# Performance work log

Hardware: AMD Instinct MI355X
Metric: run time of the kernel (lower is better)

## Reference

```python
import jax, jax.numpy as jnp
import numpy as np

N_NODES = 100000
N_EDGES = 3200000
IN_FEATS = 512
HIDDEN = 256
N_CLASSES = 64
NITER = 10
HALT_BIAS_INIT = 3.0


def setup_inputs() -> dict:
    key = jax.random.key(0)
    ks = jax.random.split(key, 8)
    x = jax.random.normal(ks[0], (N_NODES, IN_FEATS), dtype=jnp.float32)
    edge_index = jax.random.randint(ks[1], (2, N_EDGES), 0, N_NODES, dtype=jnp.int64)
    # Linear layers: layers[0]: in->hidden, layers[1]: hidden->classes, halt: classes->1
    W0 = jax.random.normal(ks[2], (IN_FEATS, HIDDEN), dtype=jnp.float32) / np.sqrt(IN_FEATS)
    b0 = jnp.zeros((HIDDEN,), dtype=jnp.float32)
    W1 = jax.random.normal(ks[3], (HIDDEN, N_CLASSES), dtype=jnp.float32) / np.sqrt(HIDDEN)
    b1 = jnp.zeros((N_CLASSES,), dtype=jnp.float32)
    Wh = jax.random.normal(ks[4], (N_CLASSES, 1), dtype=jnp.float32) / np.sqrt(N_CLASSES)
    bh = jnp.full((1,), HALT_BIAS_INIT, dtype=jnp.float32)
    return {"x": x, "edge_index": edge_index, "edge_dropout": 0,
            "W0": W0, "b0": b0, "W1": W1, "b1": b1, "Wh": Wh, "bh": bh}


def reference(x, edge_index, edge_dropout, W0, b0, W1, b1, Wh, bh):
    N = x.shape[0]
    # MLP encoder (eval mode: dropout is identity)
    h = jax.nn.relu(x @ W0 + b0)
    h = h @ W1 + b1                                   # [N, C]

    # gcn_norm with self-loops (edge_dropout=0 in eval => identical every iter)
    loops = jnp.arange(N, dtype=edge_index.dtype)
    row = jnp.concatenate([edge_index[0], loops])     # source
    col = jnp.concatenate([edge_index[1], loops])     # target (aggregation index)
    deg = jax.ops.segment_sum(jnp.ones_like(col, dtype=h.dtype), col, num_segments=N)
    dinv = jnp.where(deg > 0, deg ** -0.5, 0.0)
    norm = dinv[row] * dinv[col]                      # [E+N]

    def step(ph, _):
        msg = norm[:, None] * ph[row]                 # gather + scale, [E+N, C]
        ph2 = jax.ops.segment_sum(msg, col, num_segments=N)  # scatter_add
        logit = jnp.clip(ph2 @ Wh + bh, -10.0, 10.0)  # [N, 1]
        return ph2, (ph2, logit)

    _, (props, logits) = jax.lax.scan(step, h, None, length=NITER)
    outputs = jnp.concatenate([h[None], props], axis=0)       # [niter+1, N, C]
    halting_logits = jnp.transpose(logits[:, :, 0])           # [N, niter]

    lam = jax.nn.sigmoid(halting_logits)
    remain = jnp.cumprod(1.0 - lam, axis=1)                   # inclusive
    remain_excl = jnp.concatenate([jnp.ones((N, 1), lam.dtype), remain[:, :-1]], axis=1)
    p = lam * remain_excl
    p = p.at[:, -1].add(remain[:, -1])                        # leftover mass to last step
    return outputs, p, halting_logits
```

## Files before the change

kernel.cpp:

```cpp
#include <hip/hip_runtime.h>
#include <hip/hip_bf16.h>

#define N_NODES  100000
#define N_EDGES  3200000
#define IN_FEATS 512
#define HIDDEN   256
#define N_CLASSES 64
#define NITER    10

#define SCAN_NB  49

#define OUT_P_OFF  ((size_t)(NITER + 1) * N_NODES * N_CLASSES)
#define OUT_HL_OFF (OUT_P_OFF + (size_t)N_NODES * NITER)

#define WS_META_INTS (4 * N_NODES + 128)
#define WS_CSR_OFF   ((size_t)WS_META_INTS * 4)
#define WS_W0F_OFF   (WS_CSR_OFF + (size_t)2 * N_EDGES * 4)
#define WS_W1F_OFF   (WS_W0F_OFF + 262144)
#define WS_SH0_OFF   (WS_W1F_OFF + 32768)
#define WS_SH1_OFF   (WS_SH0_OFF + (size_t)N_NODES * 64 * 2)
#define WS_NEED_W    (WS_SH0_OFF)
#define WS_NEED_BF   (WS_SH1_OFF + (size_t)N_NODES * 64 * 2)

typedef _Float16 f16x8 __attribute__((ext_vector_type(8)));
typedef _Float16 f16x4 __attribute__((ext_vector_type(4)));
typedef float    f32x4 __attribute__((ext_vector_type(4)));

__device__ __forceinline__ float bflo(unsigned v) { return __uint_as_float(v << 16); }
__device__ __forceinline__ float bfhi(unsigned v) { return __uint_as_float(v & 0xffff0000u); }
__device__ __forceinline__ unsigned short f2bf(float f) {
    unsigned u = __float_as_uint(f);
    return (unsigned short)((u + 0x7fffu + ((u >> 16) & 1u)) >> 16);
}

__global__ void k_detect(const int* ei, int* flag) {
    if (threadIdx.x == 0 && blockIdx.x == 0) {
        int is64 = 1;
        for (int k = 0; k < 128; ++k) {
            if (ei[2 * k + 1] != 0) { is64 = 0; break; }
        }
        *flag = is64;
    }
}

__device__ __forceinline__ int edge_row(const void* ei, int is64, int e) {
    return is64 ? (int)((const long long*)ei)[e] : ((const int*)ei)[e];
}
__device__ __forceinline__ int edge_col(const void* ei, int is64, int e) {
    return is64 ? (int)((const long long*)ei)[(size_t)N_EDGES + e]
                : ((const int*)ei)[(size_t)N_EDGES + e];
}

__global__ void k_count(const void* ei, const int* flag, int* cnt) {
    int e = blockIdx.x * 256 + threadIdx.x;
    if (e >= N_EDGES) return;
    int is64 = *flag;
    atomicAdd(&cnt[edge_col(ei, is64, e)], 1);
}

__global__ __launch_bounds__(256) void k_scan1(const int* cnt, int* part) {
    __shared__ int sd[256];
    int b = blockIdx.x, t = threadIdx.x;
    int s = 0;
    for (int j = t; j < 2048; j += 256) {
        int idx = b * 2048 + j;
        if (idx < N_NODES) s += cnt[idx];
    }
    sd[t] = s;
    __syncthreads();
    for (int o = 128; o > 0; o >>= 1) {
        if (t < o) sd[t] += sd[t + o];
        __syncthreads();
    }
    if (t == 0) part[b] = sd[0];
}

__global__ __launch_bounds__(256) void k_scan2(int* part, int* offs) {
    __shared__ int sd[256];
    int t = threadIdx.x;
    sd[t] = (t < SCAN_NB) ? part[t] : 0;
    __syncthreads();
    for (int o = 1; o < 256; o <<= 1) {
        int add = (t >= o) ? sd[t - o] : 0;
        __syncthreads();
        sd[t] += add;
        __syncthreads();
    }
    if (t < SCAN_NB) part[t] = (t == 0) ? 0 : sd[t - 1];
    if (t == 0) offs[N_NODES] = N_EDGES;
}

__global__ __launch_bounds__(256) void k_scan3(const int* cnt, const int* part, int* offs) {
    __shared__ int sd[256];
    int b = blockIdx.x, t = threadIdx.x;
    int base = b * 2048 + t * 8;
    int local[8];
    int s = 0;
#pragma unroll
    for (int j = 0; j < 8; ++j) {
        int idx = base + j;
        int v = (idx < N_NODES) ? cnt[idx] : 0;
        local[j] = s;
        s += v;
    }
    sd[t] = s;
    __syncthreads();
    for (int o = 1; o < 256; o <<= 1) {
        int add = (t >= o) ? sd[t - o] : 0;
        __syncthreads();
        sd[t] += add;
        __syncthreads();
    }
    int tbase = part[b] + ((t == 0) ? 0 : sd[t - 1]);
#pragma unroll
    for (int j = 0; j < 8; ++j) {
        int idx = base + j;
        if (idx < N_NODES) offs[idx] = tbase + local[j];
    }
}

__global__ void k_dinv(const int* cnt, float* dinv) {
    int i = blockIdx.x * 256 + threadIdx.x;
    if (i >= N_NODES) return;
    dinv[i] = rsqrtf((float)(cnt[i] + 1));
}

__global__ void k_fill(const void* ei, const int* flag,
                       const int* offs, int* cursor, int* csr) {
    int e = blockIdx.x * 256 + threadIdx.x;
    if (e >= N_EDGES) return;
    int is64 = *flag;
    int r = edge_row(ei, is64, e);
    int c = edge_col(ei, is64, e);
    int pos = offs[c] + atomicAdd(&cursor[c], 1);
    csr[pos] = r << 7;
}

__global__ void k_prep_w(const float* __restrict__ W0, const float* __restrict__ W1,
                         _Float16* __restrict__ W0f, _Float16* __restrict__ W1f) {
    int id = blockIdx.x * 256 + threadIdx.x;
    if (id < 16384) {
        int l = id & 63, c = (id >> 6) & 15, kkg = id >> 10;
        int n = c * 16 + (l & 15);
        int kb = kkg * 32 + ((l >> 4) * 8);
        f16x8 v;
#pragma unroll
        for (int j = 0; j < 8; ++j) v[j] = (_Float16)W0[(size_t)(kb + j) * HIDDEN + n];
        *(f16x8*)&W0f[(size_t)id * 8] = v;
    } else if (id < 16384 + 2048) {
        int id2 = id - 16384;
        int l = id2 & 63, c = (id2 >> 6) & 3, kkg = id2 >> 8;
        int n = c * 16 + (l & 15);
        int kb = kkg * 32 + ((l >> 4) * 8);
        f16x8 v;
#pragma unroll
        for (int j = 0; j < 8; ++j) v[j] = (_Float16)W1[(size_t)(kb + j) * N_CLASSES + n];
        *(f16x8*)&W1f[(size_t)id2 * 8] = v;
    }
}

#define EBM 64
#define XS_STRIDE 72
#define H1_STRIDE 264
#define XS0   0
#define XS1   9216
#define WST0  18432
#define WST1  34816
#define W2ST0 34816
#define W2ST1 38912
__global__ __launch_bounds__(256) void k_encoder_mfma(
        const float* __restrict__ x, const _Float16* __restrict__ W0f,
        const float* __restrict__ b0, const _Float16* __restrict__ W1f,
        const float* __restrict__ b1, float* __restrict__ out,
        const float* __restrict__ dinv,
        unsigned short* __restrict__ shadow, int write_shadow) {
    __shared__ char smem[51200];
    const int t = threadIdx.x;
    const int w = t >> 6, l = t & 63;
    const int g = l >> 4, r15 = l & 15;
    const int row0 = blockIdx.x * EBM;
    const int c4 = t & 15;
    const int srow0 = t >> 4;

    f32x4 acc[16];
#pragma unroll
    for (int c = 0; c < 16; ++c) acc[c] = (f32x4){0.f, 0.f, 0.f, 0.f};

    float4 xld[4];
    f16x8 wld[4];
#pragma unroll
    for (int q = 0; q < 4; ++q) {
        int grow = row0 + q * 16 + srow0;
        if (grow >= N_NODES) grow = N_NODES - 1;
        xld[q] = *(const float4*)&x[(size_t)grow * IN_FEATS + c4 * 4];
    }
#pragma unroll
    for (int q = 0; q < 4; ++q) wld[q] = *(const f16x8*)&W0f[(size_t)(q * 256 + t) * 8];
#pragma unroll
    for (int q = 0; q < 4; ++q) {
        f16x4 hv = {(_Float16)xld[q].x, (_Float16)xld[q].y, (_Float16)xld[q].z, (_Float16)xld[q].w};
        *(f16x4*)(smem + XS0 + ((q * 16 + srow0) * XS_STRIDE + c4 * 4) * 2) = hv;
    }
#pragma unroll
    for (int q = 0; q < 4; ++q)
        *(f16x8*)(smem + WST0 + (q * 256 + t) * 16) = wld[q];
    __syncthreads();

    for (int kkg = 0; kkg < 16; ++kkg) {
        const int kc = kkg >> 1, kk = kkg & 1;
        if (kkg < 15) {
#pragma unroll
            for (int q = 0; q < 4; ++q)
                wld[q] = *(const f16x8*)&W0f[(size_t)((kkg + 1) * 1024 + q * 256 + t) * 8];
        }
        if (kk == 0 && kc < 7) {
#pragma unroll
            for (int q = 0; q < 4; ++q) {
                int grow = row0 + q * 16 + srow0;
                if (grow >= N_NODES) grow = N_NODES - 1;
                xld[q] = *(const float4*)&x[(size_t)grow * IN_FEATS + (kc + 1) * 64 + c4 * 4];
            }
        }
        const char* xbase = smem + ((kc & 1) ? XS1 : XS0);
        const char* wbase = smem + ((kkg & 1) ? WST1 : WST0);
        f16x8 af = *(const f16x8*)(xbase + ((w * 16 + r15) * XS_STRIDE + kk * 32 + g * 8) * 2);
#pragma unroll
        for (int c = 0; c < 16; ++c) {
            f16x8 bf = *(const f16x8*)(wbase + ((c << 6) | l) * 16);
            acc[c] = __builtin_amdgcn_mfma_f32_16x16x32_f16(af, bf, acc[c], 0, 0, 0);
        }
        if (kkg < 15) {
            char* wdst = smem + ((kkg & 1) ? WST0 : WST1);
#pragma unroll
            for (int q = 0; q < 4; ++q)
                *(f16x8*)(wdst + (q * 256 + t) * 16) = wld[q];
        }
        if (kk == 1 && kc < 7) {
            char* xdst = smem + ((kc & 1) ? XS0 : XS1);
#pragma unroll
            for (int q = 0; q < 4; ++q) {
                f16x4 hv = {(_Float16)xld[q].x, (_Float16)xld[q].y, (_Float16)xld[q].z, (_Float16)xld[q].w};
                *(f16x4*)(xdst + ((q * 16 + srow0) * XS_STRIDE + c4 * 4) * 2) = hv;
            }
        }
        __syncthreads();
    }

    f16x8 w2ld = *(const f16x8*)&W1f[(size_t)t * 8];
#pragma unroll
    for (int c = 0; c < 16; ++c) {
        float bb = b0[c * 16 + r15];
#pragma unroll
        for (int i = 0; i < 4; ++i) {
            int row = w * 16 + g * 4 + i;
            *(_Float16*)(smem + (row * H1_STRIDE + c * 16 + r15) * 2) =
                (_Float16)fmaxf(acc[c][i] + bb, 0.f);
        }
    }
    *(f16x8*)(smem + W2ST0 + t * 16) = w2ld;
    __syncthreads();

    f32x4 acc2[4];
#pragma unroll
    for (int c = 0; c < 4; ++c) acc2[c] = (f32x4){0.f, 0.f, 0.f, 0.f};
    for (int kkg = 0; kkg < 8; ++kkg) {
        if (kkg < 7) w2ld = *(const f16x8*)&W1f[(size_t)((kkg + 1) * 256 + t) * 8];
        const char* wbase = smem + ((kkg & 1) ? W2ST1 : W2ST0);
        f16x8 af = *(const f16x8*)(smem + ((w * 16 + r15) * H1_STRIDE + kkg * 32 + g * 8) * 2);
#pragma unroll
        for (int c = 0; c < 4; ++c) {
            f16x8 bf = *(const f16x8*)(wbase + ((c << 6) | l) * 16);
            acc2[c] = __builtin_amdgcn_mfma_f32_16x16x32_f16(af, bf, acc2[c], 0, 0, 0);
        }
        if (kkg < 7)
            *(f16x8*)(smem + ((kkg & 1) ? W2ST0 : W2ST1) + t * 16) = w2ld;
        __syncthreads();
    }
#pragma unroll
    for (int c = 0; c < 4; ++c) {
        float bb = b1[c * 16 + r15];
#pragma unroll
        for (int i = 0; i < 4; ++i) {
            int row = row0 + w * 16 + g * 4 + i;
            if (row < N_NODES) {
                float v = acc2[c][i] + bb;
                int col = c * 16 + r15;
                out[(size_t)row * 64 + col] = v;
                if (write_shadow)
                    shadow[(size_t)row * 64 + col] = f2bf(dinv[row] * v);
            }
        }
    }
}

__global__ __launch_bounds__(256) void k_encoder(const float* __restrict__ x,
        const float* __restrict__ W0, const float* __restrict__ b0,
        const float* __restrict__ W1, const float* __restrict__ b1,
        float* __restrict__ out) {
    __shared__ float xsh[32][128];
    __shared__ float h1s[32][HIDDEN + 1];
    const int t = threadIdx.x;
    const int rg = t >> 6;
    const int cg = t & 63;
    const size_t row0 = (size_t)blockIdx.x * 32;
    float acc[8][4];
#pragma unroll
    for (int i = 0; i < 8; ++i)
        acc[i][0] = acc[i][1] = acc[i][2] = acc[i][3] = 0.f;
    for (int kc = 0; kc < 4; ++kc) {
        __syncthreads();
#pragma unroll
        for (int q = 0; q < 4; ++q) {
            int idx = t + q * 256;
            int r = idx >> 5, pos = idx & 31;
            *(float4*)&xsh[r][pos * 4] =
                *(const float4*)&x[(row0 + r) * IN_FEATS + kc * 128 + pos * 4];
        }
        __syncthreads();
        for (int kk = 0; kk < 128; kk += 4) {
            float4 xv[8];
#pragma unroll
            for (int i = 0; i < 8; ++i) xv[i] = *(const float4*)&xsh[rg * 8 + i][kk];
#pragma unroll
            for (int j = 0; j < 4; ++j) {
                float4 wv = *(const float4*)&W0[(size_t)(kc * 128 + kk + j) * HIDDEN + cg * 4];
#pragma unroll
                for (int i = 0; i < 8; ++i) {
                    float xj = (&xv[i].x)[j];
                    acc[i][0] = fmaf(xj, wv.x, acc[i][0]);
                    acc[i][1] = fmaf(xj, wv.y, acc[i][1]);
                    acc[i][2] = fmaf(xj, wv.z, acc[i][2]);
                    acc[i][3] = fmaf(xj, wv.w, acc[i][3]);
                }
            }
        }
    }
    float4 bb = *(const float4*)&b0[cg * 4];
#pragma unroll
    for (int i = 0; i < 8; ++i) {
        int r = rg * 8 + i;
        h1s[r][cg * 4 + 0] = fmaxf(acc[i][0] + bb.x, 0.f);
        h1s[r][cg * 4 + 1] = fmaxf(acc[i][1] + bb.y, 0.f);
        h1s[r][cg * 4 + 2] = fmaxf(acc[i][2] + bb.z, 0.f);
        h1s[r][cg * 4 + 3] = fmaxf(acc[i][3] + bb.w, 0.f);
    }
    __syncthreads();
    float a2[8];
#pragma unroll
    for (int i = 0; i < 8; ++i) a2[i] = 0.f;
    for (int k = 0; k < HIDDEN; ++k) {
        float wv = W1[(size_t)k * N_CLASSES + cg];
#pragma unroll
        for (int i = 0; i < 8; ++i) a2[i] = fmaf(h1s[rg * 8 + i][k], wv, a2[i]);
    }
    float bv = b1[cg];
#pragma unroll
    for (int i = 0; i < 8; ++i)
        out[(row0 + rg * 8 + i) * N_CLASSES + cg] = a2[i] + bv;
}

__global__ __launch_bounds__(256) void k_prop_s(
        const unsigned short* __restrict__ pin_s, float* __restrict__ pout,
        unsigned short* __restrict__ pout_s, const int* __restrict__ offs,
        const int* __restrict__ csr, const float* __restrict__ dinv,
        const float* __restrict__ Wh, const float* __restrict__ bh,
        float* __restrict__ hl, int t) {
    int node = (blockIdx.x * 256 + threadIdx.x) >> 5;
    if (node >= N_NODES) return;
    int hlane = threadIdx.x & 31;
    int base = threadIdx.x & 32;
    const char* gbase = (const char*)pin_s + hlane * 4;
    unsigned own = *(const unsigned*)(gbase + ((size_t)node << 7));
    float a0 = bflo(own), a1 = bfhi(own);
    float c0 = 0.f, c1 = 0.f;
    int e0 = offs[node], e1 = offs[node + 1];
    for (int eb = e0; eb < e1; eb += 32) {
        int n = e1 - eb; if (n > 32) n = 32;
        int idx = eb + hlane;
        int ew = csr[idx < e1 ? idx : e1 - 1];
        int j = 0;
        for (; j + 16 <= n; j += 16) {
            unsigned v[16];
#pragma unroll
            for (int q = 0; q < 16; ++q) {
                int s = __shfl(ew, base + j + q, 64);
                v[q] = *(const unsigned*)(gbase + s);
            }
#pragma unroll
            for (int q = 0; q < 16; ++q) {
                if (q & 1) { c0 += bflo(v[q]); c1 += bfhi(v[q]); }
                else       { a0 += bflo(v[q]); a1 += bfhi(v[q]); }
            }
        }
        for (; j + 8 <= n; j += 8) {
            unsigned v[8];
#pragma unroll
            for (int q = 0; q < 8; ++q) {
                int s = __shfl(ew, base + j + q, 64);
                v[q] = *(const unsigned*)(gbase + s);
            }
#pragma unroll
            for (int q = 0; q < 8; ++q) {
                if (q & 1) { c0 += bflo(v[q]); c1 += bfhi(v[q]); }
                else       { a0 += bflo(v[q]); a1 += bfhi(v[q]); }
            }
        }
        for (; j < n; ++j) {
            int s = __shfl(ew, base + j, 64);
            unsigned v = *(const unsigned*)(gbase + s);
            a0 += bflo(v);
            a1 += bfhi(v);
        }
    }
    float di = dinv[node];
    float fa = di * (a0 + c0), fb = di * (a1 + c1);
    *(float2*)&pout[(size_t)node * 64 + hlane * 2] = make_float2(fa, fb);
    *(unsigned*)&pout_s[(size_t)node * 64 + hlane * 2] =
        (unsigned)f2bf(di * fa) | ((unsigned)f2bf(di * fb) << 16);
    float2 wh = *(const float2*)&Wh[hlane * 2];
    float s = fa * wh.x + fb * wh.y;
#pragma unroll
    for (int o = 16; o > 0; o >>= 1) s += __shfl_xor(s, o, 64);
    if (hlane == 0) {
        float lg = s + bh[0];
        lg = fminf(10.0f, fmaxf(-10.0f, lg));
        hl[(size_t)node * NITER + t] = lg;
    }
}

__global__ __launch_bounds__(256) void k_prop(const float* __restrict__ pin,
        float* __restrict__ pout, const int* __restrict__ offs,
        const int* __restrict__ csr, const float* __restrict__ dinv,
        const float* __restrict__ Wh, const float* __restrict__ bh,
        float* __restrict__ hl, int t) {
    int wid = (blockIdx.x * blockDim.x + threadIdx.x) >> 6;
    int lane = threadIdx.x & 63;
    if (wid >= N_NODES) return;
    float di = dinv[wid];
    float a[4];
    a[0] = di * di * pin[(size_t)wid * 64 + lane];
    a[1] = a[2] = a[3] = 0.f;
    int e0 = offs[wid], e1 = offs[wid + 1];
    for (int eb = e0; eb < e1; eb += 64) {
        int n = e1 - eb; if (n > 64) n = 64;
        int idx = eb + lane;
        int ew = csr[idx < e1 ? idx : e1 - 1];
        int j = 0;
        for (; j + 8 <= n; j += 8) {
            float v[8], w[8];
#pragma unroll
            for (int q = 0; q < 8; ++q) {
                int r = __shfl(ew, j + q, 64) >> 7;
                w[q] = dinv[r] * di;
                v[q] = pin[(size_t)r * 64 + lane];
            }
#pragma unroll
            for (int q = 0; q < 8; ++q) a[q & 3] = fmaf(w[q], v[q], a[q & 3]);
        }
        for (; j < n; ++j) {
            int r = __shfl(ew, j, 64) >> 7;
            a[0] = fmaf(dinv[r] * di, pin[(size_t)r * 64 + lane], a[0]);
        }
    }
    float acc = (a[0] + a[1]) + (a[2] + a[3]);
    pout[(size_t)wid * 64 + lane] = acc;
    float s = acc * Wh[lane];
#pragma unroll
    for (int o = 32; o > 0; o >>= 1) s += __shfl_xor(s, o, 64);
    if (lane == 0) {
        float lg = s + bh[0];
        lg = fminf(10.0f, fmaxf(-10.0f, lg));
        hl[(size_t)wid * NITER + t] = lg;
    }
}

__global__ void k_p(const float* __restrict__ hl, float* __restrict__ p) {
    int i = blockIdx.x * 256 + threadIdx.x;
    if (i >= N_NODES) return;
    float remain = 1.0f;
    float pv[NITER];
#pragma unroll
    for (int t = 0; t < NITER; ++t) {
        float lg = hl[(size_t)i * NITER + t];
        float lam = 1.0f / (1.0f + expf(-lg));
        pv[t] = lam * remain;
        remain *= (1.0f - lam);
    }
    pv[NITER - 1] += remain;
#pragma unroll
    for (int t = 0; t < NITER; ++t) p[(size_t)i * NITER + t] = pv[t];
}

extern "C" void kernel_launch(void* const* d_in, const int* in_sizes, int n_in,
                              void* d_out, int out_size, void* d_ws, size_t ws_size,
                              hipStream_t stream) {
    const float* x  = (const float*)d_in[0];
    const void*  ei = d_in[1];
    const float* W0 = (const float*)d_in[3];
    const float* b0 = (const float*)d_in[4];
    const float* W1 = (const float*)d_in[5];
    const float* b1 = (const float*)d_in[6];
    const float* Wh = (const float*)d_in[7];
    const float* bh = (const float*)d_in[8];
    float* out = (float*)d_out;

    int* ws_i   = (int*)d_ws;
    int* cnt    = ws_i;
    int* offs   = ws_i + N_NODES;
    int* cursor = ws_i + 2 * N_NODES + 2;
    int* part   = ws_i + 3 * N_NODES + 2;
    int* flag   = ws_i + 3 * N_NODES + 66;
    float* dinv = (float*)(ws_i + 3 * N_NODES + 128);
    int* csr    = (int*)((char*)d_ws + WS_CSR_OFF);
    _Float16* W0f = (_Float16*)((char*)d_ws + WS_W0F_OFF);
    _Float16* W1f = (_Float16*)((char*)d_ws + WS_W1F_OFF);
    unsigned short* sh0 = (unsigned short*)((char*)d_ws + WS_SH0_OFF);
    unsigned short* sh1 = (unsigned short*)((char*)d_ws + WS_SH1_OFF);

    const int use_w  = ws_size >= WS_NEED_W;
    const int use_bf = ws_size >= WS_NEED_BF;

    hipMemsetAsync(d_ws, 0, (size_t)(3 * N_NODES + 128) * 4, stream);
    k_detect<<<1, 64, 0, stream>>>((const int*)ei, flag);
    k_count<<<(N_EDGES + 255) / 256, 256, 0, stream>>>(ei, flag, cnt);
    k_scan1<<<SCAN_NB, 256, 0, stream>>>(cnt, part);
    k_scan2<<<1, 256, 0, stream>>>(part, offs);
    k_scan3<<<SCAN_NB, 256, 0, stream>>>(cnt, part, offs);
    k_dinv<<<(N_NODES + 255) / 256, 256, 0, stream>>>(cnt, dinv);
    k_fill<<<(N_EDGES + 255) / 256, 256, 0, stream>>>(ei, flag, offs, cursor, csr);

    if (use_w) {
        k_prep_w<<<72, 256, 0, stream>>>(W0, W1, W0f, W1f);
        k_encoder_mfma<<<(N_NODES + EBM - 1) / EBM, 256, 0, stream>>>(
            x, W0f, b0, W1f, b1, out, dinv, sh0, use_bf);
    } else {
        k_encoder<<<N_NODES / 32, 256, 0, stream>>>(x, W0, b0, W1, b1, out);
    }

    float* hl = out + OUT_HL_OFF;
    if (use_bf) {
        for (int it = 0; it < NITER; ++it) {
            const unsigned short* pin_s = (it & 1) ? sh1 : sh0;
            unsigned short* pout_s      = (it & 1) ? sh0 : sh1;
            float* pout = out + (size_t)(it + 1) * N_NODES * N_CLASSES;
            k_prop_s<<<((size_t)N_NODES * 32 + 255) / 256, 256, 0, stream>>>(
                pin_s, pout, pout_s, offs, csr, dinv, Wh, bh, hl, it);
        }
    } else {
        for (int it = 0; it < NITER; ++it) {
            const float* pin = out + (size_t)it * N_NODES * N_CLASSES;
            float* pout      = out + (size_t)(it + 1) * N_NODES * N_CLASSES;
            k_prop<<<((size_t)N_NODES * 64 + 255) / 256, 256, 0, stream>>>(
                pin, pout, offs, csr, dinv, Wh, bh, hl, it);
        }
    }
    k_p<<<(N_NODES + 255) / 256, 256, 0, stream>>>(hl, out + OUT_P_OFF);
}
```

Measured before the change: 992.2 us.

## Partition CSR fill by destination range and use nontemporal edge loads

The CSR fill kernel is restructured so that blockIdx&7 picks one of eight destination-node ranges. Each block group scans all edges but scatters only those whose column falls in its range, which is meant to localise the atomic cursor updates and csr writes to a narrower address region per group. Edge index loads in count and fill are switched to nontemporal loads to avoid polluting cache. The cost is reading the column array eight times.

```diff
diff --git a/kernel.cpp b/kernel.cpp
--- a/kernel.cpp
+++ b/kernel.cpp
@@ -50,12 +50,20 @@
     return is64 ? (int)((const long long*)ei)[(size_t)N_EDGES + e]
                 : ((const int*)ei)[(size_t)N_EDGES + e];
 }
+__device__ __forceinline__ int edge_row_nt(const void* ei, int is64, int e) {
+    return is64 ? (int)__builtin_nontemporal_load((const long long*)ei + e)
+                : __builtin_nontemporal_load((const int*)ei + e);
+}
+__device__ __forceinline__ int edge_col_nt(const void* ei, int is64, int e) {
+    return is64 ? (int)__builtin_nontemporal_load((const long long*)ei + (size_t)N_EDGES + e)
+                : __builtin_nontemporal_load((const int*)ei + (size_t)N_EDGES + e);
+}
 
 __global__ void k_count(const void* ei, const int* flag, int* cnt) {
     int e = blockIdx.x * 256 + threadIdx.x;
     if (e >= N_EDGES) return;
     int is64 = *flag;
-    atomicAdd(&cnt[edge_col(ei, is64, e)], 1);
+    atomicAdd(&cnt[edge_col_nt(ei, is64, e)], 1);
 }
 
 __global__ __launch_bounds__(256) void k_scan1(const int* cnt, int* part) {
@@ -125,15 +133,23 @@
     dinv[i] = rsqrtf((float)(cnt[i] + 1));
 }
 
-__global__ void k_fill(const void* ei, const int* flag,
-                       const int* offs, int* cursor, int* csr) {
-    int e = blockIdx.x * 256 + threadIdx.x;
-    if (e >= N_EDGES) return;
-    int is64 = *flag;
-    int r = edge_row(ei, is64, e);
-    int c = edge_col(ei, is64, e);
-    int pos = offs[c] + atomicAdd(&cursor[c], 1);
-    csr[pos] = r << 7;
+#define FILL_GRID 3200
+__global__ __launch_bounds__(256) void k_fill_part(const void* ei, const int* flag,
+        const int* offs, int* cursor, int* csr) {
+    const int g = blockIdx.x & 7;
+    const int bi = blockIdx.x >> 3;
+    const int lo = g * (N_NODES / 8);
+    const int hi = lo + (N_NODES / 8);
+    const int is64 = *flag;
+    const int stride = (FILL_GRID >> 3) * 256;
+    for (int e = bi * 256 + threadIdx.x; e < N_EDGES; e += stride) {
+        int c = edge_col_nt(ei, is64, e);
+        if (c >= lo && c < hi) {
+            int r = edge_row_nt(ei, is64, e);
+            int pos = offs[c] + atomicAdd(&cursor[c], 1);
+            csr[pos] = r << 7;
+        }
+    }
 }
 
 __global__ void k_prep_w(const float* __restrict__ W0, const float* __restrict__ W1,
@@ -527,7 +543,7 @@
     k_scan2<<<1, 256, 0, stream>>>(part, offs);
     k_scan3<<<SCAN_NB, 256, 0, stream>>>(cnt, part, offs);
     k_dinv<<<(N_NODES + 255) / 256, 256, 0, stream>>>(cnt, dinv);
-    k_fill<<<(N_EDGES + 255) / 256, 256, 0, stream>>>(ei, flag, offs, cursor, csr);
+    k_fill_part<<<FILL_GRID, 256, 0, stream>>>(ei, flag, offs, cursor, csr);
 
     if (use_w) {
         k_prep_w<<<72, 256, 0, stream>>>(W0, W1, W0f, W1f);
```

Result: no change. 1.002 ms (+1.0%).
